# Performance work log

Hardware: AMD Instinct MI355X
Metric: run time of the kernel (lower is better)

## Reference

```python
import jax, jax.numpy as jnp
import numpy as np
import math

N_HEADS = 12
K1 = 20
K2 = 20


def _pair(hidden, mask4, H, k1, k2):
    # hidden: [b, L, D]; mask4: [b, 1, L, L]
    b, L, D = hidden.shape
    d = D // H
    h = hidden.reshape(b, L, H, d).transpose(0, 2, 1, 3)  # [b,H,L,d]
    scores = jnp.einsum('bhid,bhjd->bhij', h, h) / math.sqrt(d)  # [b,H,L,L]
    scores = scores * mask4
    att = jax.nn.softmax(scores + (1.0 - mask4) * -10000.0, axis=-1) * mask4
    g_score = att.sum(axis=(1, 2))  # [b,L]
    _, g_top = jax.lax.top_k(g_score, k1)  # [b,k1]
    loc = att.sum(axis=1) * (1.0 - jnp.eye(L, dtype=att.dtype))  # zero diagonal
    _, l_top = jax.lax.top_k(loc, k2)  # [b,L,k2]
    idx = jnp.broadcast_to(g_top[:, :, None], (b, k1, k2))
    l_top = jnp.take_along_axis(l_top, idx, axis=1)  # [b,k1,k2]
    return scores, g_top, l_top


def _triplet(hidden, mask, g_top, l_top):
    # hidden: [b,L,D]; mask: [b,L]; g_top: [b,k1]; l_top: [b,k1,k2]; n_heads=1
    b, L, D = hidden.shape
    k1, k2 = l_top.shape[1], l_top.shape[2]
    h = hidden[:, None]  # [b,1,L,D]
    idx1 = jnp.broadcast_to(g_top[:, None, :, None], (b, 1, k1, D))
    h1 = jnp.take_along_axis(h, idx1, axis=2)  # [b,1,k1,D]
    sd = h1[:, :, :, None, :] - h[:, :, None, :, :]  # [b,1,k1,L,D]
    idx2 = jnp.broadcast_to(l_top[:, None, :, :, None], (b, 1, k1, k2, D))
    sd = jnp.take_along_axis(sd, idx2, axis=3)  # [b,1,k1,k2,D]
    nrm = jnp.linalg.norm(sd, axis=-1, keepdims=True)
    nsd = sd / jnp.maximum(nrm, 1e-12)  # F.normalize(p=2, eps=1e-12)
    angle = jnp.einsum('bhijd,bhikd->bhijk', nsd, nsd)  # [b,1,k1,k2,k2]
    m1 = jnp.take_along_axis(mask, g_top, axis=1)  # [b,k1]
    me = (m1[:, :, None] + mask[:, None, :])[:, None, :, :, None]  # [b,1,k1,L,1]
    idx3 = jnp.broadcast_to(l_top[:, None, :, :, None], (b, 1, k1, k2, 1))
    me = jnp.take_along_axis(me, idx3, axis=3)  # [b,1,k1,k2,1]
    amask = (me * me.swapaxes(-2, -1) == 4.0).astype(angle.dtype)  # both valid
    nz = (angle != 0).astype(angle.dtype) * (1.0 - jnp.eye(k2, dtype=angle.dtype))
    amask = amask * nz
    return angle * amask, amask


def setup_inputs() -> dict:
    key = jax.random.key(0)
    k1, k2 = jax.random.split(key)
    b, L, D = 8, 512, 768
    return {
        's_rep': jax.random.normal(k1, (b, L, D), dtype=jnp.float32),
        't_rep': jax.random.normal(k2, (b, L, D), dtype=jnp.float32),
        'attention_mask': jnp.ones((b, L), dtype=jnp.float32),
    }


def reference(s_rep, t_rep, attention_mask):
    b, L, D = s_rep.shape
    k1 = min(K1, L)
    k2 = min(K2, L)
    mext = attention_mask[:, :, None] * attention_mask[:, None, :]  # [b,L,L]
    mask4 = mext[:, None, :, :]  # broadcasts over heads
    s_pair, s_g, s_l = _pair(s_rep, mask4, N_HEADS, k1, k2)
    t_rep_ng = jax.lax.stop_gradient(t_rep)
    t_pair, t_g, t_l = _pair(t_rep_ng, mask4, N_HEADS, k1, k2)
    t_pair = jax.lax.stop_gradient(t_pair)
    denom = N_HEADS * jnp.sum(mext)
    loss_pair = jnp.sum((s_pair - t_pair) ** 2) / denom
    s_angle, s_mask = _triplet(s_rep, attention_mask, t_g, t_l)
    t_angle, t_mask = _triplet(t_rep_ng, attention_mask, t_g, t_l)
    t_angle = jax.lax.stop_gradient(t_angle)
    diff = s_angle - t_angle
    ad = jnp.abs(diff)
    sl1 = jnp.where(ad < 1.0, 0.5 * diff * diff, ad - 0.5)  # smooth_l1, beta=1
    loss_triplet = jnp.sum(sl1) / jnp.sum(s_mask)
    return loss_pair + loss_triplet
```

## Files before the change

kernel.cpp:

```cpp
#include <hip/hip_runtime.h>
#include <hip/hip_bf16.h>
#include <math.h>

#define Bn 8
#define Ln 512
#define Dn 768
#define NHn 12
#define DHn 64
#define K1n 20
#define K2n 20
#define BST 72
#define TROWS 64

#define WS_ACC    0
#define WS_GSCORE 64
#define WS_GTOP   16448
#define WS_LOCP   17152
#define WS_SBF    3949312
#define WS_TBF    10240768

typedef __attribute__((ext_vector_type(8))) short bf16x8;
typedef __attribute__((ext_vector_type(4))) float f32x4;

__device__ inline unsigned short f2bf(float x) {
  __hip_bfloat16 h = __float2bfloat16(x);
  return *reinterpret_cast<unsigned short*>(&h);
}
__device__ inline float bf2f(unsigned short u) {
  return __uint_as_float(((unsigned int)u) << 16);
}

__global__ __launch_bounds__(256) void prep_bf16_kernel(
    const float* __restrict__ s, const float* __restrict__ t,
    unsigned short* __restrict__ sbf, unsigned short* __restrict__ tbf,
    float* __restrict__ g_score, int* __restrict__ accw) {
  int tid = threadIdx.x;
  if (blockIdx.x == 0) {
    if (tid < 16) accw[tid] = 0;
    for (int i = tid; i < Bn * Ln; i += 256) g_score[i] = 0.0f;
  }
  int gid = blockIdx.x * 256 + tid;
  int f = gid * 4;
  int col = f % Dn;
  int rb = f / Dn;
  int row = rb & (Ln - 1);
  int b = rb >> 9;
  int h = col >> 6;
  int k = col & 63;
  size_t dst = (((size_t)(b * NHn + h) * Ln + row) * DHn + k);
  float4 vs = *(const float4*)(s + f);
  float4 vt = *(const float4*)(t + f);
  ushort4 us, ut;
  us.x = f2bf(vs.x); us.y = f2bf(vs.y); us.z = f2bf(vs.z); us.w = f2bf(vs.w);
  ut.x = f2bf(vt.x); ut.y = f2bf(vt.y); ut.z = f2bf(vt.z); ut.w = f2bf(vt.w);
  *(ushort4*)(sbf + dst) = us;
  *(ushort4*)(tbf + dst) = ut;
}

__global__ __launch_bounds__(256) void pairA_kernel(
    const unsigned short* __restrict__ sbf, const unsigned short* __restrict__ tbf,
    const float* __restrict__ mask, float* __restrict__ g_score,
    double* __restrict__ acc) {
  const int b = blockIdx.x & 7;
  const int r = blockIdx.x >> 3;
  const int it = r / NHn;
  const int h = r - it * NHn;
  const int tid = threadIdx.x;
  const int w = tid >> 6;
  const int lane = tid & 63;
  const int lr = lane & 15, lg = lane >> 4;

  __shared__ unsigned short Bs[2][TROWS * BST];
  __shared__ unsigned short Bt[2][TROWS * BST];
  __shared__ float Mcol[Ln];
  __shared__ float gcol[Ln];
  __shared__ float wred[4];

  const int s_r0 = tid >> 3;
  const int s_r1 = s_r0 + 32;
  const int s_c = (tid & 7) * 8;

  for (int j = tid; j < Ln; j += 256) {
    Mcol[j] = mask[b * Ln + j];
    gcol[j] = 0.0f;
  }

  const size_t hb = (size_t)(b * NHn + h) * Ln;
  const int rw = it * 64 + w * 16;
  const unsigned short* pas = sbf + (hb + rw + lr) * DHn + lg * 8;
  const unsigned short* pat = tbf + (hb + rw + lr) * DHn + lg * 8;
  bf16x8 sa0 = *(const bf16x8*)pas;
  bf16x8 sa1 = *(const bf16x8*)(pas + 32);
  bf16x8 ta0 = *(const bf16x8*)pat;
  bf16x8 ta1 = *(const bf16x8*)(pat + 32);

  {
    bf16x8 v0 = *(const bf16x8*)(sbf + (hb + s_r0) * DHn + s_c);
    bf16x8 v1 = *(const bf16x8*)(sbf + (hb + s_r1) * DHn + s_c);
    bf16x8 u0 = *(const bf16x8*)(tbf + (hb + s_r0) * DHn + s_c);
    bf16x8 u1 = *(const bf16x8*)(tbf + (hb + s_r1) * DHn + s_c);
    *(bf16x8*)&Bs[0][s_r0 * BST + s_c] = v0;
    *(bf16x8*)&Bs[0][s_r1 * BST + s_c] = v1;
    *(bf16x8*)&Bt[0][s_r0 * BST + s_c] = u0;
    *(bf16x8*)&Bt[0][s_r1 * BST + s_c] = u1;
  }
  __syncthreads();

  float mrow[4];
  #pragma unroll
  for (int q = 0; q < 4; ++q) mrow[q] = Mcol[rw + lg * 4 + q];

  const f32x4 zero4 = {0.0f, 0.0f, 0.0f, 0.0f};
  float lpair = 0.0f;
  float rsum[4] = {0.0f, 0.0f, 0.0f, 0.0f};

  #pragma unroll 1
  for (int t = 0; t < 8; ++t) {
    const int cur = t & 1;
    bf16x8 v0, v1, u0, u1;
    if (t < 7) {
      const int jn = (t + 1) * TROWS;
      v0 = *(const bf16x8*)(sbf + (hb + jn + s_r0) * DHn + s_c);
      v1 = *(const bf16x8*)(sbf + (hb + jn + s_r1) * DHn + s_c);
      u0 = *(const bf16x8*)(tbf + (hb + jn + s_r0) * DHn + s_c);
      u1 = *(const bf16x8*)(tbf + (hb + jn + s_r1) * DHn + s_c);
    }
    #pragma unroll
    for (int c = 0; c < 4; ++c) {
      const int jl = c * 16;
      const int j0 = t * TROWS + jl;
      const unsigned short* pbs = &Bs[cur][(jl + lr) * BST + lg * 8];
      const unsigned short* pbt = &Bt[cur][(jl + lr) * BST + lg * 8];
      bf16x8 sb0 = *(const bf16x8*)pbs;
      bf16x8 sb1 = *(const bf16x8*)(pbs + 32);
      bf16x8 tb0 = *(const bf16x8*)pbt;
      bf16x8 tb1 = *(const bf16x8*)(pbt + 32);
      f32x4 sacc = __builtin_amdgcn_mfma_f32_16x16x32_bf16(sa0, sb0, zero4, 0, 0, 0);
      sacc = __builtin_amdgcn_mfma_f32_16x16x32_bf16(sa1, sb1, sacc, 0, 0, 0);
      f32x4 tacc = __builtin_amdgcn_mfma_f32_16x16x32_bf16(ta0, tb0, zero4, 0, 0, 0);
      tacc = __builtin_amdgcn_mfma_f32_16x16x32_bf16(ta1, tb1, tacc, 0, 0, 0);
      const float mj = Mcol[j0 + lr];
      #pragma unroll
      for (int q = 0; q < 4; ++q) {
        const float mm = mrow[q] * mj;
        const float ss = sacc[q] * 0.125f * mm;
        const float st = tacc[q] * 0.125f * mm;
        const float d = ss - st;
        lpair += d * d;
        rsum[q] += __expf(st + (1.0f - mm) * (-10000.0f));
      }
    }
    if (t < 7) {
      const int nxt = cur ^ 1;
      *(bf16x8*)&Bs[nxt][s_r0 * BST + s_c] = v0;
      *(bf16x8*)&Bs[nxt][s_r1 * BST + s_c] = v1;
      *(bf16x8*)&Bt[nxt][s_r0 * BST + s_c] = u0;
      *(bf16x8*)&Bt[nxt][s_r1 * BST + s_c] = u1;
    }
    __syncthreads();
  }

  #pragma unroll
  for (int o = 1; o < 16; o <<= 1) {
    #pragma unroll
    for (int q = 0; q < 4; ++q) rsum[q] += __shfl_xor(rsum[q], o, 64);
  }
  float rscale[4];
  #pragma unroll
  for (int q = 0; q < 4; ++q)
    rscale[q] = mrow[q] / fmaxf(rsum[q], 1e-30f);

  {
    bf16x8 u0 = *(const bf16x8*)(tbf + (hb + s_r0) * DHn + s_c);
    bf16x8 u1 = *(const bf16x8*)(tbf + (hb + s_r1) * DHn + s_c);
    *(bf16x8*)&Bt[0][s_r0 * BST + s_c] = u0;
    *(bf16x8*)&Bt[0][s_r1 * BST + s_c] = u1;
  }
  __syncthreads();

  #pragma unroll 1
  for (int t = 0; t < 8; ++t) {
    const int cur = t & 1;
    bf16x8 u0, u1;
    if (t < 7) {
      const int jn = (t + 1) * TROWS;
      u0 = *(const bf16x8*)(tbf + (hb + jn + s_r0) * DHn + s_c);
      u1 = *(const bf16x8*)(tbf + (hb + jn + s_r1) * DHn + s_c);
    }
    #pragma unroll
    for (int c = 0; c < 4; ++c) {
      const int jl = c * 16;
      const int j0 = t * TROWS + jl;
      const unsigned short* pbt = &Bt[cur][(jl + lr) * BST + lg * 8];
      bf16x8 tb0 = *(const bf16x8*)pbt;
      bf16x8 tb1 = *(const bf16x8*)(pbt + 32);
      f32x4 tacc = __builtin_amdgcn_mfma_f32_16x16x32_bf16(ta0, tb0, zero4, 0, 0, 0);
      tacc = __builtin_amdgcn_mfma_f32_16x16x32_bf16(ta1, tb1, tacc, 0, 0, 0);
      const float mj = Mcol[j0 + lr];
      float pc = 0.0f;
      #pragma unroll
      for (int q = 0; q < 4; ++q) {
        const float mm = mrow[q] * mj;
        const float st = tacc[q] * 0.125f * mm;
        const float e = __expf(st + (1.0f - mm) * (-10000.0f));
        pc += e * rscale[q];
      }
      pc += __shfl_xor(pc, 16, 64);
      pc += __shfl_xor(pc, 32, 64);
      if (lg == 0) atomicAdd(&gcol[j0 + lr], pc);
    }
    if (t < 7) {
      const int nxt = cur ^ 1;
      *(bf16x8*)&Bt[nxt][s_r0 * BST + s_c] = u0;
      *(bf16x8*)&Bt[nxt][s_r1 * BST + s_c] = u1;
    }
    __syncthreads();
  }

  #pragma unroll
  for (int o = 1; o < 64; o <<= 1) lpair += __shfl_xor(lpair, o, 64);
  if (lane == 0) wred[w] = lpair;
  __syncthreads();

  if (tid == 0) {
    atomicAdd(&acc[0], (double)((wred[0] + wred[1]) + (wred[2] + wred[3])));
  }
  {
    const int j0 = tid, j1 = tid + 256;
    atomicAdd(&g_score[b * Ln + j0], gcol[j0] * Mcol[j0]);
    atomicAdd(&g_score[b * Ln + j1], gcol[j1] * Mcol[j1]);
  }
}

__global__ __launch_bounds__(256, 4) void pairB_kernel(
    const unsigned short* __restrict__ tbf, const float* __restrict__ mask,
    const float* __restrict__ g_score, int* __restrict__ g_top,
    float* __restrict__ loc_part) {
  const int b = blockIdx.x & 7;
  const int h = blockIdx.x >> 3;
  const int tid = threadIdx.x;
  const int w = tid >> 6, lane = tid & 63;
  const int lr = lane & 15, lg = lane >> 4;
  const int cw = w * 128;

  __shared__ int gidx[32];
  __shared__ float mrow_s[32];
  __shared__ float rscale_s[32];
  __shared__ float redsum[4][32];
  __shared__ float McolB[Ln];
  __shared__ unsigned short es[32][Ln + 8];

  for (int j = tid; j < Ln; j += 256) McolB[j] = mask[b * Ln + j];
  if (w == 1 && lane < 32 - K1n) gidx[K1n + lane] = 0;
  if (w == 0) {
    float v[8];
    #pragma unroll
    for (int q = 0; q < 8; ++q) v[q] = g_score[b * Ln + q * 64 + lane];
    for (int r = 0; r < K1n; ++r) {
      float bv = v[0]; int bq = 0;
      #pragma unroll
      for (int q = 1; q < 8; ++q) if (v[q] > bv) { bv = v[q]; bq = q; }
      int bj = bq * 64 + lane;
      #pragma unroll
      for (int o = 1; o < 64; o <<= 1) {
        float ov = __shfl_xor(bv, o, 64);
        int oj = __shfl_xor(bj, o, 64);
        if (ov > bv || (ov == bv && oj < bj)) { bv = ov; bj = oj; }
      }
      if (lane == 0) {
        gidx[r] = bj;
        if (h == 0) g_top[b * K1n + r] = bj;
      }
      const int wq = bj >> 6, wl = bj & 63;
      #pragma unroll
      for (int q = 0; q < 8; ++q)
        if (q == wq && lane == wl) v[q] = -3.0e38f;
    }
  }
  __syncthreads();
  if (tid < 32) mrow_s[tid] = (tid < K1n) ? McolB[gidx[tid]] : 0.0f;
  __syncthreads();

  const size_t hb = (size_t)(b * NHn + h) * Ln;
  bf16x8 ta[2][2];
  #pragma unroll
  for (int rt = 0; rt < 2; ++rt) {
    const unsigned short* p = tbf + (hb + gidx[rt * 16 + lr]) * DHn + lg * 8;
    ta[rt][0] = *(const bf16x8*)p;
    ta[rt][1] = *(const bf16x8*)(p + 32);
  }
  const f32x4 zero4 = {0.0f, 0.0f, 0.0f, 0.0f};
  float rsum[2][4] = {{0, 0, 0, 0}, {0, 0, 0, 0}};
  #pragma unroll 1
  for (int ct = 0; ct < 8; ++ct) {
    const int j0 = cw + ct * 16;
    const unsigned short* pb = tbf + (hb + j0 + lr) * DHn + lg * 8;
    bf16x8 tb0 = *(const bf16x8*)pb;
    bf16x8 tb1 = *(const bf16x8*)(pb + 32);
    const float mj = McolB[j0 + lr];
    #pragma unroll
    for (int rt = 0; rt < 2; ++rt) {
      f32x4 tacc = __builtin_amdgcn_mfma_f32_16x16x32_bf16(ta[rt][0], tb0, zero4, 0, 0, 0);
      tacc = __builtin_amdgcn_mfma_f32_16x16x32_bf16(ta[rt][1], tb1, tacc, 0, 0, 0);
      #pragma unroll
      for (int q = 0; q < 4; ++q) {
        const int ri = rt * 16 + lg * 4 + q;
        const float mm = mrow_s[ri] * mj;
        const float st = tacc[q] * 0.125f * mm;
        const float e = __expf(st + (1.0f - mm) * (-10000.0f));
        rsum[rt][q] += e;
        es[ri][j0 + lr] = f2bf(e);
      }
    }
  }
  #pragma unroll
  for (int o = 1; o < 16; o <<= 1) {
    #pragma unroll
    for (int rt = 0; rt < 2; ++rt)
      #pragma unroll
      for (int q = 0; q < 4; ++q) rsum[rt][q] += __shfl_xor(rsum[rt][q], o, 64);
  }
  if (lr == 0) {
    #pragma unroll
    for (int rt = 0; rt < 2; ++rt)
      #pragma unroll
      for (int q = 0; q < 4; ++q) redsum[w][rt * 16 + lg * 4 + q] = rsum[rt][q];
  }
  __syncthreads();
  if (tid < 32) {
    const float fs = redsum[0][tid] + redsum[1][tid] + redsum[2][tid] + redsum[3][tid];
    rscale_s[tid] = mrow_s[tid] / fmaxf(fs, 1e-30f);
  }
  __syncthreads();
  float* lp = loc_part + (size_t)(h * Bn + b) * K1n * Ln;
  for (int idx = tid; idx < K1n * Ln; idx += 256) {
    const int ri = idx >> 9, j = idx & (Ln - 1);
    const float e = bf2f(es[ri][j]);
    lp[idx] = e * rscale_s[ri] * McolB[j];
  }
}

#define TPW (Dn + 16)

__global__ __launch_bounds__(512, 1) void triplet_kernel(
    const float* __restrict__ s_rep, const float* __restrict__ t_rep,
    const float* __restrict__ mask, const int* __restrict__ g_top,
    const float* __restrict__ loc_part, double* __restrict__ acc,
    unsigned int* __restrict__ done_cnt, float* __restrict__ out) {
  const int blk = blockIdx.x, tid = threadIdx.x;
  const int b = blk / K1n, i1 = blk % K1n;
  const int w = tid >> 6, lane = tid & 63;
  const int lr = lane & 15, lg = lane >> 4;

  __shared__ unsigned short NS[32][TPW];
  __shared__ unsigned short NT[32][TPW];
  __shared__ float locsum[Ln];
  __shared__ float gsr[Dn], gtr[Dn];
  __shared__ float G[2][K2n][K2n + 1];
  __shared__ float ssqL[40];
  __shared__ float rsinv[40];
  __shared__ int lidx[K2n];
  __shared__ float fl2[K2n];
  __shared__ float sred[8], cred[8];
  __shared__ int is_last;
  __shared__ float red[8];

  const int g = g_top[b * K1n + i1];

  {
    const int j = tid;
    float sv = 0.0f;
    #pragma unroll
    for (int hh = 0; hh < NHn; ++hh)
      sv += loc_part[((size_t)(hh * Bn + b) * K1n + i1) * Ln + j];
    locsum[j] = (j == g) ? 0.0f : sv;
  }
  {
    const float* pgs = s_rep + (size_t)(b * Ln + g) * Dn;
    const float* pgt = t_rep + (size_t)(b * Ln + g) * Dn;
    if (tid < 192) {
      *(float4*)&gsr[tid * 4] = *(const float4*)&pgs[tid * 4];
    } else if (tid < 384) {
      const int q4 = tid - 192;
      *(float4*)&gtr[q4 * 4] = *(const float4*)&pgt[q4 * 4];
    }
  }
  __syncthreads();

  if (w == 0) {
    float v[8];
    #pragma unroll
    for (int q = 0; q < 8; ++q) v[q] = locsum[q * 64 + lane];
    for (int r = 0; r < K2n; ++r) {
      float bv = v[0]; int bq = 0;
      #pragma unroll
      for (int q = 1; q < 8; ++q) if (v[q] > bv) { bv = v[q]; bq = q; }
      int bj = bq * 64 + lane;
      #pragma unroll
      for (int o = 1; o < 64; o <<= 1) {
        float ov = __shfl_xor(bv, o, 64);
        int oj = __shfl_xor(bj, o, 64);
        if (ov > bv || (ov == bv && oj < bj)) { bv = ov; bj = oj; }
      }
      if (lane == 0) lidx[r] = bj;
      const int wq = bj >> 6, wl = bj & 63;
      #pragma unroll
      for (int q = 0; q < 8; ++q)
        if (q == wq && lane == wl) v[q] = -3.0e38f;
    }
  }
  __syncthreads();
  if (tid < K2n)
    fl2[tid] = (mask[b * Ln + g] + mask[b * Ln + lidx[tid]] == 2.0f) ? 1.0f : 0.0f;

  {
    float ssq_acc[5] = {0.0f, 0.0f, 0.0f, 0.0f, 0.0f};
    #pragma unroll
    for (int i = 0; i < 15; ++i) {
      const int rl = i / 3;
      const int q = i % 3;
      const int rt = w * 5 + rl;
      const bool isS = rt < 20;
      const int row = isS ? rt : rt - 20;
      const int c = q * 256 + lane * 4;
      const float* src = (isS ? s_rep : t_rep) +
                         (size_t)(b * Ln + lidx[row]) * Dn + c;
      float4 x = *(const float4*)src;
      const float* gp = isS ? gsr : gtr;
      float4 a = *(const float4*)&gp[c];
      float4 d = make_float4(a.x - x.x, a.y - x.y, a.z - x.z, a.w - x.w);
      ushort4 u;
      u.x = f2bf(d.x); u.y = f2bf(d.y); u.z = f2bf(d.z); u.w = f2bf(d.w);
      if (isS) *(ushort4*)&NS[row][c] = u;
      else     *(ushort4*)&NT[row][c] = u;
      ssq_acc[rl] += d.x * d.x + d.y * d.y + d.z * d.z + d.w * d.w;
    }
    #pragma unroll
    for (int rl = 0; rl < 5; ++rl) {
      float v = ssq_acc[rl];
      #pragma unroll
      for (int o = 1; o < 64; o <<= 1) v += __shfl_xor(v, o, 64);
      if (lane == 0) ssqL[w * 5 + rl] = v;
    }
  }
  __syncthreads();
  if (tid < 40) rsinv[tid] = 1.0f / fmaxf(sqrtf(ssqL[tid]), 1e-12f);
  __syncthreads();

  for (int idx = tid; idx < 40 * 192; idx += 512) {
    const int rt = idx / 192;
    const int c = (idx - rt * 192) * 4;
    const float sc = rsinv[rt];
    unsigned short* N = (rt < 20) ? &NS[rt][c] : &NT[rt - 20][c];
    ushort4 u = *(ushort4*)N;
    u.x = f2bf(bf2f(u.x) * sc); u.y = f2bf(bf2f(u.y) * sc);
    u.z = f2bf(bf2f(u.z) * sc); u.w = f2bf(bf2f(u.w) * sc);
    *(ushort4*)N = u;
  }
  __syncthreads();

  {
    const int ts = w & 1;
    const int qr = w >> 2;
    const int qc = (w >> 1) & 1;
    const unsigned short (*N)[TPW] = ts ? NT : NS;
    f32x4 acc4 = {0.0f, 0.0f, 0.0f, 0.0f};
    #pragma unroll
    for (int ks = 0; ks < 24; ++ks) {
      const int kk = ks * 32 + lg * 8;
      bf16x8 a8 = *(const bf16x8*)&N[qr * 16 + lr][kk];
      bf16x8 b8 = *(const bf16x8*)&N[qc * 16 + lr][kk];
      acc4 = __builtin_amdgcn_mfma_f32_16x16x32_bf16(a8, b8, acc4, 0, 0, 0);
    }
    #pragma unroll
    for (int q = 0; q < 4; ++q) {
      const int j2 = qr * 16 + lg * 4 + q;
      const int k2 = qc * 16 + lr;
      if (j2 < K2n && k2 < K2n) G[ts][j2][k2] = acc4[q];
    }
  }
  __syncthreads();

  float psum = 0.0f, pcnt = 0.0f;
  if (tid < K2n * K2n) {
    const int j2 = tid / K2n, k2 = tid - j2 * K2n;
    if (j2 != k2) {
      const float am = fl2[j2] * fl2[k2];
      const float sv0 = G[0][j2][k2];
      const float tv0 = G[1][j2][k2];
      const bool smv = (am != 0.0f) && (sv0 != 0.0f);
      const bool tmv = (am != 0.0f) && (tv0 != 0.0f);
      const float sv = smv ? sv0 : 0.0f;
      const float tv = tmv ? tv0 : 0.0f;
      const float d = sv - tv;
      const float ad = fabsf(d);
      psum = (ad < 1.0f) ? 0.5f * d * d : (ad - 0.5f);
      pcnt = smv ? 1.0f : 0.0f;
    }
  }
  #pragma unroll
  for (int o = 1; o < 64; o <<= 1) {
    psum += __shfl_xor(psum, o, 64);
    pcnt += __shfl_xor(pcnt, o, 64);
  }
  if (lane == 0) { sred[w] = psum; cred[w] = pcnt; }
  __syncthreads();
  if (tid == 0) {
    float ps = 0.0f, pcs = 0.0f;
    #pragma unroll
    for (int i = 0; i < 8; ++i) { ps += sred[i]; pcs += cred[i]; }
    atomicAdd(&acc[1], (double)ps);
    atomicAdd(&acc[2], (double)pcs);
    __threadfence();
    const unsigned int done = atomicAdd(done_cnt, 1u);
    is_last = (done == (unsigned int)(Bn * K1n - 1)) ? 1 : 0;
  }
  __syncthreads();

  if (is_last) {
    double sm = 0.0;
    for (int bb = 0; bb < Bn; ++bb) {
      float p = (tid < Ln) ? mask[bb * Ln + tid] : 0.0f;
      #pragma unroll
      for (int o = 1; o < 64; o <<= 1) p += __shfl_xor(p, o, 64);
      __syncthreads();
      if ((tid & 63) == 0) red[tid >> 6] = p;
      __syncthreads();
      if (tid == 0) {
        float rs = 0.0f;
        #pragma unroll
        for (int i = 0; i < 8; ++i) rs += red[i];
        sm += (double)rs * (double)rs;
      }
    }
    __syncthreads();
    if (tid == 0) {
      const double a0 = atomicAdd(&acc[0], 0.0);
      const double a1 = atomicAdd(&acc[1], 0.0);
      const double a2 = atomicAdd(&acc[2], 0.0);
      const double lp = a0 / ((double)NHn * sm);
      const double lt = a1 / a2;
      out[0] = (float)(lp + lt);
    }
  }
}

extern "C" void kernel_launch(void* const* d_in, const int* in_sizes, int n_in,
                              void* d_out, int out_size, void* d_ws, size_t ws_size,
                              hipStream_t stream) {
  const float* s_rep = (const float*)d_in[0];
  const float* t_rep = (const float*)d_in[1];
  const float* mask  = (const float*)d_in[2];
  float* out = (float*)d_out;

  char* w = (char*)d_ws;
  double* acc      = (double*)(w + WS_ACC);
  unsigned int* done_cnt = (unsigned int*)(w + WS_ACC + 48);
  float* g_score   = (float*)(w + WS_GSCORE);
  int* g_top       = (int*)(w + WS_GTOP);
  float* loc_part  = (float*)(w + WS_LOCP);
  unsigned short* sbf = (unsigned short*)(w + WS_SBF);
  unsigned short* tbf = (unsigned short*)(w + WS_TBF);

  prep_bf16_kernel<<<Bn * Ln * Dn / 4 / 256, 256, 0, stream>>>(
      s_rep, t_rep, sbf, tbf, g_score, (int*)(w + WS_ACC));
  pairA_kernel<<<Bn * NHn * (Ln / 64), 256, 0, stream>>>(sbf, tbf, mask, g_score, acc);
  pairB_kernel<<<Bn * NHn, 256, 0, stream>>>(tbf, mask, g_score, g_top, loc_part);
  triplet_kernel<<<Bn * K1n, 512, 0, stream>>>(s_rep, t_rep, mask, g_top, loc_part,
                                               acc, done_cnt, out);
}
```

Measured before the change: 102.5 us.

## Split triplet kernel into top-k, gram, and finalize kernels

```diff
diff --git a/kernel.cpp b/kernel.cpp
--- a/kernel.cpp
+++ b/kernel.cpp
@@ -15,9 +15,10 @@
 #define WS_ACC    0
 #define WS_GSCORE 64
 #define WS_GTOP   16448
-#define WS_LOCP   17152
-#define WS_SBF    3949312
-#define WS_TBF    10240768
+#define WS_LTOP   17152
+#define WS_LOCP   29952
+#define WS_SBF    3962112
+#define WS_TBF    10253568
 
 typedef __attribute__((ext_vector_type(8))) short bf16x8;
 typedef __attribute__((ext_vector_type(4))) float f32x4;
@@ -340,13 +341,47 @@
   }
 }
 
+__global__ __launch_bounds__(64) void topk_l_kernel(
+    const float* __restrict__ loc_part, const int* __restrict__ g_top,
+    int* __restrict__ l_top) {
+  const int blk = blockIdx.x, lane = threadIdx.x;
+  const int b = blk / K1n, i1 = blk % K1n;
+  const int g = g_top[b * K1n + i1];
+  float v[8];
+  #pragma unroll
+  for (int q = 0; q < 8; ++q) {
+    const int j = q * 64 + lane;
+    float sv = 0.0f;
+    #pragma unroll
+    for (int hh = 0; hh < NHn; ++hh)
+      sv += loc_part[((size_t)(hh * Bn + b) * K1n + i1) * Ln + j];
+    v[q] = (j == g) ? 0.0f : sv;
+  }
+  for (int r = 0; r < K2n; ++r) {
+    float bv = v[0]; int bq = 0;
+    #pragma unroll
+    for (int q = 1; q < 8; ++q) if (v[q] > bv) { bv = v[q]; bq = q; }
+    int bj = bq * 64 + lane;
+    #pragma unroll
+    for (int o = 1; o < 64; o <<= 1) {
+      float ov = __shfl_xor(bv, o, 64);
+      int oj = __shfl_xor(bj, o, 64);
+      if (ov > bv || (ov == bv && oj < bj)) { bv = ov; bj = oj; }
+    }
+    if (lane == 0) l_top[(b * K1n + i1) * K2n + r] = bj;
+    const int wq = bj >> 6, wl = bj & 63;
+    #pragma unroll
+    for (int q = 0; q < 8; ++q)
+      if (q == wq && lane == wl) v[q] = -3.0e38f;
+  }
+}
+
 #define TPW (Dn + 16)
 
-__global__ __launch_bounds__(512, 1) void triplet_kernel(
+__global__ __launch_bounds__(512, 1) void gram_kernel(
     const float* __restrict__ s_rep, const float* __restrict__ t_rep,
     const float* __restrict__ mask, const int* __restrict__ g_top,
-    const float* __restrict__ loc_part, double* __restrict__ acc,
-    unsigned int* __restrict__ done_cnt, float* __restrict__ out) {
+    const int* __restrict__ l_top, double* __restrict__ acc) {
   const int blk = blockIdx.x, tid = threadIdx.x;
   const int b = blk / K1n, i1 = blk % K1n;
   const int w = tid >> 6, lane = tid & 63;
@@ -354,7 +389,6 @@
 
   __shared__ unsigned short NS[32][TPW];
   __shared__ unsigned short NT[32][TPW];
-  __shared__ float locsum[Ln];
   __shared__ float gsr[Dn], gtr[Dn];
   __shared__ float G[2][K2n][K2n + 1];
   __shared__ float ssqL[40];
@@ -362,19 +396,9 @@
   __shared__ int lidx[K2n];
   __shared__ float fl2[K2n];
   __shared__ float sred[8], cred[8];
-  __shared__ int is_last;
-  __shared__ float red[8];
 
   const int g = g_top[b * K1n + i1];
-
-  {
-    const int j = tid;
-    float sv = 0.0f;
-    #pragma unroll
-    for (int hh = 0; hh < NHn; ++hh)
-      sv += loc_part[((size_t)(hh * Bn + b) * K1n + i1) * Ln + j];
-    locsum[j] = (j == g) ? 0.0f : sv;
-  }
+  if (tid < K2n) lidx[tid] = l_top[(b * K1n + i1) * K2n + tid];
   {
     const float* pgs = s_rep + (size_t)(b * Ln + g) * Dn;
     const float* pgt = t_rep + (size_t)(b * Ln + g) * Dn;
@@ -383,30 +407,6 @@
     } else if (tid < 384) {
       const int q4 = tid - 192;
       *(float4*)&gtr[q4 * 4] = *(const float4*)&pgt[q4 * 4];
-    }
-  }
-  __syncthreads();
-
-  if (w == 0) {
-    float v[8];
-    #pragma unroll
-    for (int q = 0; q < 8; ++q) v[q] = locsum[q * 64 + lane];
-    for (int r = 0; r < K2n; ++r) {
-      float bv = v[0]; int bq = 0;
-      #pragma unroll
-      for (int q = 1; q < 8; ++q) if (v[q] > bv) { bv = v[q]; bq = q; }
-      int bj = bq * 64 + lane;
-      #pragma unroll
-      for (int o = 1; o < 64; o <<= 1) {
-        float ov = __shfl_xor(bv, o, 64);
-        int oj = __shfl_xor(bj, o, 64);
-        if (ov > bv || (ov == bv && oj < bj)) { bv = ov; bj = oj; }
-      }
-      if (lane == 0) lidx[r] = bj;
-      const int wq = bj >> 6, wl = bj & 63;
-      #pragma unroll
-      for (int q = 0; q < 8; ++q)
-        if (q == wq && lane == wl) v[q] = -3.0e38f;
     }
   }
   __syncthreads();
@@ -511,37 +511,32 @@
     for (int i = 0; i < 8; ++i) { ps += sred[i]; pcs += cred[i]; }
     atomicAdd(&acc[1], (double)ps);
     atomicAdd(&acc[2], (double)pcs);
-    __threadfence();
-    const unsigned int done = atomicAdd(done_cnt, 1u);
-    is_last = (done == (unsigned int)(Bn * K1n - 1)) ? 1 : 0;
-  }
-  __syncthreads();
-
-  if (is_last) {
-    double sm = 0.0;
-    for (int bb = 0; bb < Bn; ++bb) {
-      float p = (tid < Ln) ? mask[bb * Ln + tid] : 0.0f;
-      #pragma unroll
-      for (int o = 1; o < 64; o <<= 1) p += __shfl_xor(p, o, 64);
-      __syncthreads();
-      if ((tid & 63) == 0) red[tid >> 6] = p;
-      __syncthreads();
-      if (tid == 0) {
-        float rs = 0.0f;
-        #pragma unroll
-        for (int i = 0; i < 8; ++i) rs += red[i];
-        sm += (double)rs * (double)rs;
-      }
-    }
+  }
+}
+
+__global__ void finalize_kernel(const float* __restrict__ mask,
+                                const double* __restrict__ acc, float* __restrict__ out) {
+  int tid = threadIdx.x;
+  __shared__ float red[4];
+  double sm = 0.0;
+  for (int b = 0; b < Bn; ++b) {
+    float p = 0.0f;
+    for (int i = tid; i < Ln; i += 256) p += mask[b * Ln + i];
+    #pragma unroll
+    for (int o = 1; o < 64; o <<= 1) p += __shfl_xor(p, o, 64);
+    __syncthreads();
+    if ((tid & 63) == 0) red[tid >> 6] = p;
     __syncthreads();
     if (tid == 0) {
-      const double a0 = atomicAdd(&acc[0], 0.0);
-      const double a1 = atomicAdd(&acc[1], 0.0);
-      const double a2 = atomicAdd(&acc[2], 0.0);
-      const double lp = a0 / ((double)NHn * sm);
-      const double lt = a1 / a2;
-      out[0] = (float)(lp + lt);
-    }
+      float rs = red[0] + red[1] + red[2] + red[3];
+      sm += (double)rs * (double)rs;
+    }
+  }
+  __syncthreads();
+  if (tid == 0) {
+    double lp = acc[0] / ((double)NHn * sm);
+    double lt = acc[1] / acc[2];
+    out[0] = (float)(lp + lt);
   }
 }
 
@@ -555,9 +550,9 @@
 
   char* w = (char*)d_ws;
   double* acc      = (double*)(w + WS_ACC);
-  unsigned int* done_cnt = (unsigned int*)(w + WS_ACC + 48);
   float* g_score   = (float*)(w + WS_GSCORE);
   int* g_top       = (int*)(w + WS_GTOP);
+  int* l_top       = (int*)(w + WS_LTOP);
   float* loc_part  = (float*)(w + WS_LOCP);
   unsigned short* sbf = (unsigned short*)(w + WS_SBF);
   unsigned short* tbf = (unsigned short*)(w + WS_TBF);
@@ -566,6 +561,7 @@
       s_rep, t_rep, sbf, tbf, g_score, (int*)(w + WS_ACC));
   pairA_kernel<<<Bn * NHn * (Ln / 64), 256, 0, stream>>>(sbf, tbf, mask, g_score, acc);
   pairB_kernel<<<Bn * NHn, 256, 0, stream>>>(tbf, mask, g_score, g_top, loc_part);
-  triplet_kernel<<<Bn * K1n, 512, 0, stream>>>(s_rep, t_rep, mask, g_top, loc_part,
-                                               acc, done_cnt, out);
-}
+  topk_l_kernel<<<Bn * K1n, 64, 0, stream>>>(loc_part, g_top, l_top);
+  gram_kernel<<<Bn * K1n, 512, 0, stream>>>(s_rep, t_rep, mask, g_top, l_top, acc);
+  finalize_kernel<<<1, 256, 0, stream>>>(mask, acc, out);
+}
```

Measured after the change: 103.1 us. About the same (+0.6%).
